# Kernel tuning notes

Measured on AMD Instinct MI355X. Metric: run time of the kernel, lower is better.

## Reference

```python
import jax, jax.numpy as jnp
import numpy as np
from jax import lax

N = 4096      # network_size
B = 1024      # batch
AVG_DEG = 6.0 # scale-free preferential attachment adds ~3 edges/node (undirected)
N_STEPS = 10


def setup_inputs() -> dict:
    key = jax.random.key(0)
    k_in, k_adj = jax.random.split(key)
    external_input = jax.random.normal(k_in, (B, N), dtype=jnp.float32)
    # symmetric binary adjacency with average degree ~6 (stand-in for scale-free topology)
    a = jax.random.bernoulli(k_adj, AVG_DEG / N, (N, N))
    connectivity = jnp.maximum(a, a.T).astype(jnp.float32)
    connectivity = connectivity * (1.0 - jnp.eye(N, dtype=jnp.float32))  # no self-loops
    membrane_potentials = jnp.zeros((N,), dtype=jnp.float32)  # nn.Parameter init zeros
    thresholds = jnp.ones((N,), dtype=jnp.float32)            # nn.Parameter init ones
    refractory_periods = jnp.zeros((N,), dtype=jnp.float32)   # nn.Parameter init zeros
    return {
        "external_input": external_input,
        "connectivity": connectivity,
        "membrane_potentials": membrane_potentials,
        "thresholds": thresholds,
        "refractory_periods": refractory_periods,
    }


def reference(external_input, connectivity, membrane_potentials, thresholds, refractory_periods):
    b, n = external_input.shape
    v0 = membrane_potentials[None, :] + external_input          # [B, N]
    s0 = jnp.zeros((b, n), dtype=external_input.dtype)          # spikes

    def step(carry, _):
        v, s, refr = carry
        v = v + 0.1 * (s @ connectivity)                         # network input
        mask = (v > thresholds[None, :]) & (refr == 0.0)[None, :]
        new_s = mask.astype(v.dtype)
        v = jnp.where(mask, 0.0, v)                              # reset on spike
        refr = jnp.where(jnp.any(mask, axis=0), 3.0, refr)       # set refractory
        refr = jnp.clip(refr - 1.0, 0.0, 10.0)                   # decay
        v = v * 0.95                                             # leak
        return (v, new_s, refr), None

    (_, spikes, _), _ = lax.scan(step, (v0, s0, refractory_periods), None, length=N_STEPS)
    return spikes
```

## Files before the change

### kernel.cpp

```cpp
#include <hip/hip_runtime.h>
#include <stdint.h>

#define N_ 4096
#define B_ 1024
#define NSTEPS_ 10
#define DEG_SLOTS 40
#define UNR 16
#define PAD_E ((uint32_t)(N_ * B_))
#define NBLK 256
#define NCTR 16
#define FLAGI 512

#define OFF_BAR  0
#define OFF_DEG  8192
#define OFF_NBR  24576
#define OFF_SEXP 679936
#define SEXP_BUF ((N_ + 1) * B_)

__global__ __launch_bounds__(256) void build_k(const float* __restrict__ C,
                                               uint32_t* __restrict__ deg,
                                               uint32_t* __restrict__ nbr,
                                               uint32_t* __restrict__ bar,
                                               uint32_t* __restrict__ pad0,
                                               uint32_t* __restrict__ pad1) {
    __shared__ uint32_t cnt;
    int tid = threadIdx.x;
    int n = blockIdx.x;
    if (n == 0) { for (int i = tid; i < 1056; i += 256) bar[i] = 0u; }
    else if (n == 1) { pad0[tid] = 0u; }
    else if (n == 2) { pad1[tid] = 0u; }
    if (tid == 0) cnt = 0;
    __syncthreads();
    const float4* row = (const float4*)(C + (size_t)n * N_);
    for (int j4 = tid; j4 < N_ / 4; j4 += 256) {
        float4 v = row[j4];
        int base = j4 * 4;
        #pragma unroll
        for (int q = 0; q < 4; ++q) {
            float f = (q == 0) ? v.x : (q == 1) ? v.y : (q == 2) ? v.z : v.w;
            if (f != 0.0f) {
                uint32_t p = atomicAdd(&cnt, 1u);
                uint32_t m = (uint32_t)(base + q);
                if (p < DEG_SLOTS) nbr[n * DEG_SLOTS + p] = m * (uint32_t)B_;
            }
        }
    }
    __syncthreads();
    uint32_t c = min(cnt, (uint32_t)DEG_SLOTS);
    if (tid == 0) deg[n] = c;
    if (tid < DEG_SLOTS && (uint32_t)tid >= c)
        nbr[n * DEG_SLOTS + tid] = PAD_E;
}

__device__ __forceinline__ void gbar(uint32_t* bar, uint32_t phase) {
    __syncthreads();
    int tid = threadIdx.x, bid = blockIdx.x;
    if (tid == 0)
        __hip_atomic_fetch_add(&bar[(bid & (NCTR - 1)) * 32], 1u,
                               __ATOMIC_RELAXED, __HIP_MEMORY_SCOPE_AGENT);
    if (bid == 0) {
        if (tid < NCTR) {
            uint32_t tgt = (NBLK / NCTR) * phase;
            while (__hip_atomic_load(&bar[tid * 32], __ATOMIC_RELAXED,
                                     __HIP_MEMORY_SCOPE_AGENT) < tgt)
                __builtin_amdgcn_s_sleep(2);
        }
        __syncthreads();
        if (tid == 0)
            __hip_atomic_store(&bar[FLAGI], phase,
                               __ATOMIC_RELAXED, __HIP_MEMORY_SCOPE_AGENT);
    }
    if (tid == 0) {
        while (__hip_atomic_load(&bar[FLAGI], __ATOMIC_RELAXED,
                                 __HIP_MEMORY_SCOPE_AGENT) < phase)
            __builtin_amdgcn_s_sleep(2);
        (void)__hip_atomic_load(&bar[FLAGI], __ATOMIC_ACQUIRE,
                                __HIP_MEMORY_SCOPE_AGENT);
    }
    __syncthreads();
}

__global__ __launch_bounds__(1024, 4) void persist_k(const float* __restrict__ ext,
                                                     const float* __restrict__ memb,
                                                     const float* __restrict__ thr,
                                                     const float* __restrict__ refr_in,
                                                     const uint32_t* __restrict__ deg,
                                                     const uint32_t* __restrict__ nbr,
                                                     unsigned char* __restrict__ sExp,
                                                     float* __restrict__ out,
                                                     uint32_t* bar) {
    __shared__ uint32_t s_nbr[16 * DEG_SLOTS];
    __shared__ unsigned char bt[16][1040];

    int bid = blockIdx.x;
    int n0 = bid * 16;
    int tid = threadIdx.x;
    int wv = tid >> 6, lane = tid & 63;
    int n = n0 + wv;
    int bb = lane * 16;

    if (tid < 16 * DEG_SLOTS) s_nbr[tid] = nbr[(size_t)n0 * DEG_SLOTS + tid];
    __syncthreads();

    float tn = thr[n];
    float r  = refr_in[n];
    uint32_t dg = __builtin_amdgcn_readfirstlane(deg[n]);
    const uint32_t* lst = &s_nbr[wv * DEG_SLOTS];

    float v[16];
    {
        float mb = memb[n];
        #pragma unroll
        for (int i = 0; i < 16; ++i)
            v[i] = __fadd_rn(mb, ext[(size_t)(bb + i) * N_ + n]);
    }

    uint32_t spk[4];

    {
        uint32_t nb = (r != 0.0f) ? 0u : 1u;
        #pragma unroll
        for (int dw = 0; dw < 4; ++dw) {
            int sp0 = (v[dw * 4 + 0] > tn) && nb;
            int sp1 = (v[dw * 4 + 1] > tn) && nb;
            int sp2 = (v[dw * 4 + 2] > tn) && nb;
            int sp3 = (v[dw * 4 + 3] > tn) && nb;
            spk[dw] = (uint32_t)sp0 | ((uint32_t)sp1 << 8) |
                      ((uint32_t)sp2 << 16) | ((uint32_t)sp3 << 24);
            v[dw * 4 + 0] = __fmul_rn(sp0 ? 0.0f : v[dw * 4 + 0], 0.95f);
            v[dw * 4 + 1] = __fmul_rn(sp1 ? 0.0f : v[dw * 4 + 1], 0.95f);
            v[dw * 4 + 2] = __fmul_rn(sp2 ? 0.0f : v[dw * 4 + 2], 0.95f);
            v[dw * 4 + 3] = __fmul_rn(sp3 ? 0.0f : v[dw * 4 + 3], 0.95f);
        }
        unsigned long long p0 = (unsigned long long)spk[0] | ((unsigned long long)spk[1] << 32);
        unsigned long long p1 = (unsigned long long)spk[2] | ((unsigned long long)spk[3] << 32);
        unsigned long long* dst = (unsigned long long*)(sExp + (size_t)n * B_ + bb);
        __hip_atomic_store(dst,     p0, __ATOMIC_RELAXED, __HIP_MEMORY_SCOPE_AGENT);
        __hip_atomic_store(dst + 1, p1, __ATOMIC_RELAXED, __HIP_MEMORY_SCOPE_AGENT);
        int anyl = (spk[0] | spk[1] | spk[2] | spk[3]) != 0;
        int any = (__ballot(anyl) != 0ull);
        r = any ? 3.0f : r;
        r = fminf(fmaxf(__fadd_rn(r, -1.0f), 0.0f), 10.0f);
    }
    gbar(bar, 1);

    unsigned char* sprev = sExp;
    unsigned char* snext = sExp + (size_t)SEXP_BUF;
    for (int s = 1; s < NSTEPS_; ++s) {
        uint32_t nb = (r != 0.0f) ? 0u : 1u;
        uint32_t a0 = 0, a1 = 0, a2 = 0, a3 = 0;
        #pragma unroll
        for (int j = 0; j < UNR; ++j) {
            uint32_t e = lst[j];
            uint4 d4 = *(const uint4*)(sprev + e + bb);
            a0 += d4.x; a1 += d4.y; a2 += d4.z; a3 += d4.w;
        }
        if (dg > UNR) {
            for (uint32_t j = UNR; j < dg; ++j) {
                uint32_t e = lst[j];
                uint4 d4 = *(const uint4*)(sprev + e + bb);
                a0 += d4.x; a1 += d4.y; a2 += d4.z; a3 += d4.w;
            }
        }
        uint32_t accs[4] = {a0, a1, a2, a3};
        #pragma unroll
        for (int dw = 0; dw < 4; ++dw) {
            uint32_t acc = accs[dw];
            float v0 = __fadd_rn(v[dw * 4 + 0], __fmul_rn(0.1f, (float)( acc        & 255u)));
            float v1 = __fadd_rn(v[dw * 4 + 1], __fmul_rn(0.1f, (float)((acc >>  8) & 255u)));
            float v2 = __fadd_rn(v[dw * 4 + 2], __fmul_rn(0.1f, (float)((acc >> 16) & 255u)));
            float v3 = __fadd_rn(v[dw * 4 + 3], __fmul_rn(0.1f, (float)( acc >> 24        )));
            int sp0 = (v0 > tn) && nb;
            int sp1 = (v1 > tn) && nb;
            int sp2 = (v2 > tn) && nb;
            int sp3 = (v3 > tn) && nb;
            spk[dw] = (uint32_t)sp0 | ((uint32_t)sp1 << 8) |
                      ((uint32_t)sp2 << 16) | ((uint32_t)sp3 << 24);
            if (s < NSTEPS_ - 1) {
                v[dw * 4 + 0] = __fmul_rn(sp0 ? 0.0f : v0, 0.95f);
                v[dw * 4 + 1] = __fmul_rn(sp1 ? 0.0f : v1, 0.95f);
                v[dw * 4 + 2] = __fmul_rn(sp2 ? 0.0f : v2, 0.95f);
                v[dw * 4 + 3] = __fmul_rn(sp3 ? 0.0f : v3, 0.95f);
            }
        }
        if (s < NSTEPS_ - 1) {
            unsigned long long p0 = (unsigned long long)spk[0] | ((unsigned long long)spk[1] << 32);
            unsigned long long p1 = (unsigned long long)spk[2] | ((unsigned long long)spk[3] << 32);
            unsigned long long* dst = (unsigned long long*)(snext + (size_t)n * B_ + bb);
            __hip_atomic_store(dst,     p0, __ATOMIC_RELAXED, __HIP_MEMORY_SCOPE_AGENT);
            __hip_atomic_store(dst + 1, p1, __ATOMIC_RELAXED, __HIP_MEMORY_SCOPE_AGENT);
            int anyl = (spk[0] | spk[1] | spk[2] | spk[3]) != 0;
            int any = (__ballot(anyl) != 0ull);
            r = any ? 3.0f : r;
            r = fminf(fmaxf(__fadd_rn(r, -1.0f), 0.0f), 10.0f);
            gbar(bar, (uint32_t)s + 1);
        }
        unsigned char* t = sprev; sprev = snext; snext = t;
    }

    *(uint4*)&bt[wv][bb] = make_uint4(spk[0], spk[1], spk[2], spk[3]);
    __syncthreads();
    #pragma unroll
    for (int p = 0; p < 4; ++p) {
        int i = tid + p * 1024;
        int rrow = i >> 2, c4 = (i & 3) * 4;
        float4 o;
        o.x = (float)bt[c4 + 0][rrow];
        o.y = (float)bt[c4 + 1][rrow];
        o.z = (float)bt[c4 + 2][rrow];
        o.w = (float)bt[c4 + 3][rrow];
        *(float4*)&out[(size_t)rrow * N_ + n0 + c4] = o;
    }
}

extern "C" void kernel_launch(void* const* d_in, const int* in_sizes, int n_in,
                              void* d_out, int out_size, void* d_ws, size_t ws_size,
                              hipStream_t stream) {
    const float* ext     = (const float*)d_in[0];
    const float* C       = (const float*)d_in[1];
    const float* memb    = (const float*)d_in[2];
    const float* thr     = (const float*)d_in[3];
    const float* refr_in = (const float*)d_in[4];

    char* ws = (char*)d_ws;
    uint32_t* bar    = (uint32_t*)(ws + OFF_BAR);
    uint32_t* deg    = (uint32_t*)(ws + OFF_DEG);
    uint32_t* nbr    = (uint32_t*)(ws + OFF_NBR);
    unsigned char* sExp = (unsigned char*)(ws + OFF_SEXP);
    float*    out    = (float*)d_out;

    build_k<<<dim3(N_), dim3(256), 0, stream>>>(
        C, deg, nbr, bar,
        (uint32_t*)(sExp + (size_t)N_ * B_),
        (uint32_t*)(sExp + (size_t)SEXP_BUF + (size_t)N_ * B_));

    void* args[] = {(void*)&ext, (void*)&memb, (void*)&thr, (void*)&refr_in,
                    (void*)&deg, (void*)&nbr, (void*)&sExp, (void*)&out,
                    (void*)&bar};
    hipLaunchCooperativeKernel((const void*)persist_k, dim3(NBLK), dim3(1024),
                               args, 0, stream);
}
```

Before: 147.4 us.

## Fuse adjacency list build into persistent kernel and decentralize grid barrier

```diff
diff --git a/kernel.cpp b/kernel.cpp
--- a/kernel.cpp
+++ b/kernel.cpp
@@ -9,47 +9,13 @@
 #define PAD_E ((uint32_t)(N_ * B_))
 #define NBLK 256
 #define NCTR 16
-#define FLAGI 512
 
 #define OFF_BAR  0
-#define OFF_DEG  8192
-#define OFF_NBR  24576
-#define OFF_SEXP 679936
+#define OFF_SEXP 8192
 #define SEXP_BUF ((N_ + 1) * B_)
 
-__global__ __launch_bounds__(256) void build_k(const float* __restrict__ C,
-                                               uint32_t* __restrict__ deg,
-                                               uint32_t* __restrict__ nbr,
-                                               uint32_t* __restrict__ bar,
-                                               uint32_t* __restrict__ pad0,
-                                               uint32_t* __restrict__ pad1) {
-    __shared__ uint32_t cnt;
-    int tid = threadIdx.x;
-    int n = blockIdx.x;
-    if (n == 0) { for (int i = tid; i < 1056; i += 256) bar[i] = 0u; }
-    else if (n == 1) { pad0[tid] = 0u; }
-    else if (n == 2) { pad1[tid] = 0u; }
-    if (tid == 0) cnt = 0;
-    __syncthreads();
-    const float4* row = (const float4*)(C + (size_t)n * N_);
-    for (int j4 = tid; j4 < N_ / 4; j4 += 256) {
-        float4 v = row[j4];
-        int base = j4 * 4;
-        #pragma unroll
-        for (int q = 0; q < 4; ++q) {
-            float f = (q == 0) ? v.x : (q == 1) ? v.y : (q == 2) ? v.z : v.w;
-            if (f != 0.0f) {
-                uint32_t p = atomicAdd(&cnt, 1u);
-                uint32_t m = (uint32_t)(base + q);
-                if (p < DEG_SLOTS) nbr[n * DEG_SLOTS + p] = m * (uint32_t)B_;
-            }
-        }
-    }
-    __syncthreads();
-    uint32_t c = min(cnt, (uint32_t)DEG_SLOTS);
-    if (tid == 0) deg[n] = c;
-    if (tid < DEG_SLOTS && (uint32_t)tid >= c)
-        nbr[n * DEG_SLOTS + tid] = PAD_E;
+__global__ void initbar_k(uint32_t* __restrict__ bar) {
+    for (int i = threadIdx.x; i < 512; i += 256) bar[i] = 0u;
 }
 
 __device__ __forceinline__ void gbar(uint32_t* bar, uint32_t phase) {
@@ -58,38 +24,28 @@
     if (tid == 0)
         __hip_atomic_fetch_add(&bar[(bid & (NCTR - 1)) * 32], 1u,
                                __ATOMIC_RELAXED, __HIP_MEMORY_SCOPE_AGENT);
-    if (bid == 0) {
-        if (tid < NCTR) {
-            uint32_t tgt = (NBLK / NCTR) * phase;
-            while (__hip_atomic_load(&bar[tid * 32], __ATOMIC_RELAXED,
-                                     __HIP_MEMORY_SCOPE_AGENT) < tgt)
-                __builtin_amdgcn_s_sleep(2);
-        }
-        __syncthreads();
-        if (tid == 0)
-            __hip_atomic_store(&bar[FLAGI], phase,
-                               __ATOMIC_RELAXED, __HIP_MEMORY_SCOPE_AGENT);
-    }
-    if (tid == 0) {
-        while (__hip_atomic_load(&bar[FLAGI], __ATOMIC_RELAXED,
-                                 __HIP_MEMORY_SCOPE_AGENT) < phase)
+    if (tid < NCTR) {
+        uint32_t tgt = (NBLK / NCTR) * phase;
+        while (__hip_atomic_load(&bar[tid * 32], __ATOMIC_RELAXED,
+                                 __HIP_MEMORY_SCOPE_AGENT) < tgt)
             __builtin_amdgcn_s_sleep(2);
-        (void)__hip_atomic_load(&bar[FLAGI], __ATOMIC_ACQUIRE,
+    }
+    if (tid == 0)
+        (void)__hip_atomic_load(&bar[0], __ATOMIC_ACQUIRE,
                                 __HIP_MEMORY_SCOPE_AGENT);
-    }
     __syncthreads();
 }
 
 __global__ __launch_bounds__(1024, 4) void persist_k(const float* __restrict__ ext,
+                                                     const float* __restrict__ C,
                                                      const float* __restrict__ memb,
                                                      const float* __restrict__ thr,
                                                      const float* __restrict__ refr_in,
-                                                     const uint32_t* __restrict__ deg,
-                                                     const uint32_t* __restrict__ nbr,
                                                      unsigned char* __restrict__ sExp,
                                                      float* __restrict__ out,
                                                      uint32_t* bar) {
     __shared__ uint32_t s_nbr[16 * DEG_SLOTS];
+    __shared__ uint32_t s_cnt[16];
     __shared__ unsigned char bt[16][1040];
 
     int bid = blockIdx.x;
@@ -99,12 +55,41 @@
     int n = n0 + wv;
     int bb = lane * 16;
 
-    if (tid < 16 * DEG_SLOTS) s_nbr[tid] = nbr[(size_t)n0 * DEG_SLOTS + tid];
+    if (tid < 16) s_cnt[tid] = 0u;
+    __syncthreads();
+    {
+        const float4* row = (const float4*)(C + (size_t)n * N_);
+        for (int j4 = lane; j4 < N_ / 4; j4 += 64) {
+            float4 vv = row[j4];
+            int base = j4 * 4;
+            #pragma unroll
+            for (int q = 0; q < 4; ++q) {
+                float f = (q == 0) ? vv.x : (q == 1) ? vv.y : (q == 2) ? vv.z : vv.w;
+                if (f != 0.0f) {
+                    uint32_t p = atomicAdd(&s_cnt[wv], 1u);
+                    uint32_t m = (uint32_t)(base + q);
+                    if (p < DEG_SLOTS) s_nbr[wv * DEG_SLOTS + p] = m * (uint32_t)B_;
+                }
+            }
+        }
+    }
+    if (bid == 1 && tid < 128) {
+        __hip_atomic_store((unsigned long long*)(sExp + (size_t)N_ * B_) + tid, 0ull,
+                           __ATOMIC_RELAXED, __HIP_MEMORY_SCOPE_AGENT);
+    } else if (bid == 2 && tid < 128) {
+        __hip_atomic_store((unsigned long long*)(sExp + (size_t)SEXP_BUF + (size_t)N_ * B_) + tid,
+                           0ull, __ATOMIC_RELAXED, __HIP_MEMORY_SCOPE_AGENT);
+    }
+    __syncthreads();
+    for (int i = tid; i < 16 * DEG_SLOTS; i += 1024) {
+        int rw = i / DEG_SLOTS, sl = i - rw * DEG_SLOTS;
+        if ((uint32_t)sl >= min(s_cnt[rw], (uint32_t)DEG_SLOTS)) s_nbr[i] = PAD_E;
+    }
     __syncthreads();
 
     float tn = thr[n];
     float r  = refr_in[n];
-    uint32_t dg = __builtin_amdgcn_readfirstlane(deg[n]);
+    uint32_t dg = __builtin_amdgcn_readfirstlane(min(s_cnt[wv], (uint32_t)DEG_SLOTS));
     const uint32_t* lst = &s_nbr[wv * DEG_SLOTS];
 
     float v[16];
@@ -151,13 +136,13 @@
         uint32_t a0 = 0, a1 = 0, a2 = 0, a3 = 0;
         #pragma unroll
         for (int j = 0; j < UNR; ++j) {
-            uint32_t e = lst[j];
+            uint32_t e = __builtin_amdgcn_readfirstlane(lst[j]);
             uint4 d4 = *(const uint4*)(sprev + e + bb);
             a0 += d4.x; a1 += d4.y; a2 += d4.z; a3 += d4.w;
         }
         if (dg > UNR) {
             for (uint32_t j = UNR; j < dg; ++j) {
-                uint32_t e = lst[j];
+                uint32_t e = __builtin_amdgcn_readfirstlane(lst[j]);
                 uint4 d4 = *(const uint4*)(sprev + e + bb);
                 a0 += d4.x; a1 += d4.y; a2 += d4.z; a3 += d4.w;
             }
@@ -224,19 +209,13 @@
 
     char* ws = (char*)d_ws;
     uint32_t* bar    = (uint32_t*)(ws + OFF_BAR);
-    uint32_t* deg    = (uint32_t*)(ws + OFF_DEG);
-    uint32_t* nbr    = (uint32_t*)(ws + OFF_NBR);
     unsigned char* sExp = (unsigned char*)(ws + OFF_SEXP);
     float*    out    = (float*)d_out;
 
-    build_k<<<dim3(N_), dim3(256), 0, stream>>>(
-        C, deg, nbr, bar,
-        (uint32_t*)(sExp + (size_t)N_ * B_),
-        (uint32_t*)(sExp + (size_t)SEXP_BUF + (size_t)N_ * B_));
-
-    void* args[] = {(void*)&ext, (void*)&memb, (void*)&thr, (void*)&refr_in,
-                    (void*)&deg, (void*)&nbr, (void*)&sExp, (void*)&out,
-                    (void*)&bar};
+    initbar_k<<<dim3(1), dim3(256), 0, stream>>>(bar);
+
+    void* args[] = {(void*)&ext, (void*)&C, (void*)&memb, (void*)&thr,
+                    (void*)&refr_in, (void*)&sExp, (void*)&out, (void*)&bar};
     hipLaunchCooperativeKernel((const void*)persist_k, dim3(NBLK), dim3(1024),
                                args, 0, stream);
 }
```

Result: slower. 175.0 us (+18.8%).

## Split each neuron's batch across two waves and double the persistent grid

Applied to the files above, without the earlier changes.

```diff
diff --git a/kernel.cpp b/kernel.cpp
--- a/kernel.cpp
+++ b/kernel.cpp
@@ -7,7 +7,7 @@
 #define DEG_SLOTS 40
 #define UNR 16
 #define PAD_E ((uint32_t)(N_ * B_))
-#define NBLK 256
+#define NBLK 512
 #define NCTR 16
 #define FLAGI 512
 
@@ -80,7 +80,7 @@
     __syncthreads();
 }
 
-__global__ __launch_bounds__(1024, 4) void persist_k(const float* __restrict__ ext,
+__global__ __launch_bounds__(1024, 8) void persist_k(const float* __restrict__ ext,
                                                      const float* __restrict__ memb,
                                                      const float* __restrict__ thr,
                                                      const float* __restrict__ refr_in,
@@ -89,38 +89,40 @@
                                                      unsigned char* __restrict__ sExp,
                                                      float* __restrict__ out,
                                                      uint32_t* bar) {
-    __shared__ uint32_t s_nbr[16 * DEG_SLOTS];
-    __shared__ unsigned char bt[16][1040];
+    __shared__ uint32_t s_nbr[8 * DEG_SLOTS];
+    __shared__ uint32_t s_any[16];
+    __shared__ unsigned char bt[8][1040];
 
     int bid = blockIdx.x;
-    int n0 = bid * 16;
+    int n0 = bid * 8;
     int tid = threadIdx.x;
     int wv = tid >> 6, lane = tid & 63;
-    int n = n0 + wv;
-    int bb = lane * 16;
-
-    if (tid < 16 * DEG_SLOTS) s_nbr[tid] = nbr[(size_t)n0 * DEG_SLOTS + tid];
+    int nn = wv >> 1, half = wv & 1;
+    int n = n0 + nn;
+    int bb = half * 512 + lane * 8;
+
+    if (tid < 8 * DEG_SLOTS) s_nbr[tid] = nbr[(size_t)n0 * DEG_SLOTS + tid];
     __syncthreads();
 
     float tn = thr[n];
     float r  = refr_in[n];
     uint32_t dg = __builtin_amdgcn_readfirstlane(deg[n]);
-    const uint32_t* lst = &s_nbr[wv * DEG_SLOTS];
-
-    float v[16];
+    const uint32_t* lst = &s_nbr[nn * DEG_SLOTS];
+
+    float v[8];
     {
         float mb = memb[n];
         #pragma unroll
-        for (int i = 0; i < 16; ++i)
+        for (int i = 0; i < 8; ++i)
             v[i] = __fadd_rn(mb, ext[(size_t)(bb + i) * N_ + n]);
     }
 
-    uint32_t spk[4];
+    uint32_t spk[2];
 
     {
         uint32_t nb = (r != 0.0f) ? 0u : 1u;
         #pragma unroll
-        for (int dw = 0; dw < 4; ++dw) {
+        for (int dw = 0; dw < 2; ++dw) {
             int sp0 = (v[dw * 4 + 0] > tn) && nb;
             int sp1 = (v[dw * 4 + 1] > tn) && nb;
             int sp2 = (v[dw * 4 + 2] > tn) && nb;
@@ -133,38 +135,40 @@
             v[dw * 4 + 3] = __fmul_rn(sp3 ? 0.0f : v[dw * 4 + 3], 0.95f);
         }
         unsigned long long p0 = (unsigned long long)spk[0] | ((unsigned long long)spk[1] << 32);
-        unsigned long long p1 = (unsigned long long)spk[2] | ((unsigned long long)spk[3] << 32);
-        unsigned long long* dst = (unsigned long long*)(sExp + (size_t)n * B_ + bb);
-        __hip_atomic_store(dst,     p0, __ATOMIC_RELAXED, __HIP_MEMORY_SCOPE_AGENT);
-        __hip_atomic_store(dst + 1, p1, __ATOMIC_RELAXED, __HIP_MEMORY_SCOPE_AGENT);
-        int anyl = (spk[0] | spk[1] | spk[2] | spk[3]) != 0;
-        int any = (__ballot(anyl) != 0ull);
+        __hip_atomic_store((unsigned long long*)(sExp + (size_t)n * B_ + bb), p0,
+                           __ATOMIC_RELAXED, __HIP_MEMORY_SCOPE_AGENT);
+        unsigned long long m64 = __ballot((spk[0] | spk[1]) != 0);
+        if (lane == 0) s_any[wv] = (m64 != 0ull) ? 1u : 0u;
+    }
+    gbar(bar, 1);
+    {
+        int any = (s_any[2 * nn] | s_any[2 * nn + 1]) != 0u;
         r = any ? 3.0f : r;
         r = fminf(fmaxf(__fadd_rn(r, -1.0f), 0.0f), 10.0f);
-    }
-    gbar(bar, 1);
+        __syncthreads();
+    }
 
     unsigned char* sprev = sExp;
     unsigned char* snext = sExp + (size_t)SEXP_BUF;
     for (int s = 1; s < NSTEPS_; ++s) {
         uint32_t nb = (r != 0.0f) ? 0u : 1u;
-        uint32_t a0 = 0, a1 = 0, a2 = 0, a3 = 0;
+        uint32_t a0 = 0, a1 = 0;
         #pragma unroll
         for (int j = 0; j < UNR; ++j) {
             uint32_t e = lst[j];
-            uint4 d4 = *(const uint4*)(sprev + e + bb);
-            a0 += d4.x; a1 += d4.y; a2 += d4.z; a3 += d4.w;
+            uint2 d2 = *(const uint2*)(sprev + e + bb);
+            a0 += d2.x; a1 += d2.y;
         }
         if (dg > UNR) {
             for (uint32_t j = UNR; j < dg; ++j) {
                 uint32_t e = lst[j];
-                uint4 d4 = *(const uint4*)(sprev + e + bb);
-                a0 += d4.x; a1 += d4.y; a2 += d4.z; a3 += d4.w;
+                uint2 d2 = *(const uint2*)(sprev + e + bb);
+                a0 += d2.x; a1 += d2.y;
             }
         }
-        uint32_t accs[4] = {a0, a1, a2, a3};
-        #pragma unroll
-        for (int dw = 0; dw < 4; ++dw) {
+        uint32_t accs[2] = {a0, a1};
+        #pragma unroll
+        for (int dw = 0; dw < 2; ++dw) {
             uint32_t acc = accs[dw];
             float v0 = __fadd_rn(v[dw * 4 + 0], __fmul_rn(0.1f, (float)( acc        & 255u)));
             float v1 = __fadd_rn(v[dw * 4 + 1], __fmul_rn(0.1f, (float)((acc >>  8) & 255u)));
@@ -185,25 +189,25 @@
         }
         if (s < NSTEPS_ - 1) {
             unsigned long long p0 = (unsigned long long)spk[0] | ((unsigned long long)spk[1] << 32);
-            unsigned long long p1 = (unsigned long long)spk[2] | ((unsigned long long)spk[3] << 32);
-            unsigned long long* dst = (unsigned long long*)(snext + (size_t)n * B_ + bb);
-            __hip_atomic_store(dst,     p0, __ATOMIC_RELAXED, __HIP_MEMORY_SCOPE_AGENT);
-            __hip_atomic_store(dst + 1, p1, __ATOMIC_RELAXED, __HIP_MEMORY_SCOPE_AGENT);
-            int anyl = (spk[0] | spk[1] | spk[2] | spk[3]) != 0;
-            int any = (__ballot(anyl) != 0ull);
+            __hip_atomic_store((unsigned long long*)(snext + (size_t)n * B_ + bb), p0,
+                               __ATOMIC_RELAXED, __HIP_MEMORY_SCOPE_AGENT);
+            unsigned long long m64 = __ballot((spk[0] | spk[1]) != 0);
+            if (lane == 0) s_any[wv] = (m64 != 0ull) ? 1u : 0u;
+            gbar(bar, (uint32_t)s + 1);
+            int any = (s_any[2 * nn] | s_any[2 * nn + 1]) != 0u;
             r = any ? 3.0f : r;
             r = fminf(fmaxf(__fadd_rn(r, -1.0f), 0.0f), 10.0f);
-            gbar(bar, (uint32_t)s + 1);
+            __syncthreads();
         }
         unsigned char* t = sprev; sprev = snext; snext = t;
     }
 
-    *(uint4*)&bt[wv][bb] = make_uint4(spk[0], spk[1], spk[2], spk[3]);
+    *(uint2*)&bt[nn][bb] = make_uint2(spk[0], spk[1]);
     __syncthreads();
     #pragma unroll
-    for (int p = 0; p < 4; ++p) {
+    for (int p = 0; p < 2; ++p) {
         int i = tid + p * 1024;
-        int rrow = i >> 2, c4 = (i & 3) * 4;
+        int rrow = i >> 1, c4 = (i & 1) * 4;
         float4 o;
         o.x = (float)bt[c4 + 0][rrow];
         o.y = (float)bt[c4 + 1][rrow];
```

Result: slower. 176.6 us (+19.9%).
